# Optimization experiments

Hardware: AMD Instinct MI355X
Metric: run time of the kernel (lower is better)

## Reference

```python
import jax, jax.numpy as jnp
import numpy as np

N, K, D, C, H = 200000, 256, 12, 9, 32
EPS = 1e-8


def setup_inputs() -> dict:
    key = jax.random.key(0)
    ks = jax.random.split(key, 8)
    probe_pos = jax.random.uniform(ks[0], (N, 3), dtype=jnp.float32)
    mu = jax.random.uniform(ks[1], (K, 3), dtype=jnp.float32)
    log_s = jax.random.normal(ks[2], (K, 3), dtype=jnp.float32) * 0.3 - 1.5
    # quaternions near identity (w~1) as in the torch init
    q = jax.random.normal(ks[3], (K, 4), dtype=jnp.float32) * 0.1 + jnp.array([1.0, 0.0, 0.0, 0.0], jnp.float32)
    F = jax.random.normal(ks[4], (K, D), dtype=jnp.float32) * 0.1
    W1 = jax.random.normal(ks[5], (D + 3, H), dtype=jnp.float32) / np.sqrt(D + 3).astype(np.float32)
    b1 = jnp.zeros((H,), jnp.float32)
    W2 = jax.random.normal(ks[6], (H, C), dtype=jnp.float32) / np.sqrt(H).astype(np.float32)
    b2 = jnp.zeros((C,), jnp.float32)
    return {"probe_pos": probe_pos, "mu": mu, "log_s": log_s, "q": q,
            "F": F, "W1": W1, "b1": b1, "W2": W2, "b2": b2}


def quaternion_to_rotation_matrix(q):
    # q: [K,4] (w,x,y,z) -> [K,3,3]
    q = q / (jnp.linalg.norm(q, axis=-1, keepdims=True) + EPS)
    w, x, y, z = q[..., 0], q[..., 1], q[..., 2], q[..., 3]
    r0 = jnp.stack([1 - 2 * y * y - 2 * z * z, 2 * x * y - 2 * w * z, 2 * x * z + 2 * w * y], axis=-1)
    r1 = jnp.stack([2 * x * y + 2 * w * z, 1 - 2 * x * x - 2 * z * z, 2 * y * z - 2 * w * x], axis=-1)
    r2 = jnp.stack([2 * x * z - 2 * w * y, 2 * y * z + 2 * w * x, 1 - 2 * x * x - 2 * y * y], axis=-1)
    return jnp.stack([r0, r1, r2], axis=-2)


def reference(probe_pos, mu, log_s, q, F, W1, b1, W2, b2):
    s = jnp.exp(log_s)                                   # [K,3]
    R = quaternion_to_rotation_matrix(q)                 # [K,3,3]
    s_inv_sq = 1.0 / (s ** 2 + EPS)                      # [K,3]
    # precision = R @ diag(s_inv_sq) @ R^T -> [K,3,3]
    precision = jnp.einsum('kij,kj,klj->kil', R, s_inv_sq, R)
    diff = probe_pos[:, None, :] - mu[None, :, :]        # [N,K,3]
    mahal = jnp.einsum('nki,kij,nkj->nk', diff, precision, diff)  # [N,K]
    gvals = jnp.exp(-0.5 * mahal)                        # [N,K]
    radii = 3.0 * s.max(axis=1)                          # [K]
    dist = jnp.linalg.norm(diff, axis=2)                 # [N,K]
    gvals = gvals * (dist < radii[None, :]).astype(gvals.dtype)
    weights = gvals / (gvals.sum(axis=1, keepdims=True) + EPS)    # [N,K]
    latent = weights @ F                                 # [N,D]
    mlp_in = jnp.concatenate([latent, probe_pos], axis=1)         # [N,D+3]
    h = jax.nn.relu(mlp_in @ W1 + b1)                    # [N,H]
    sh = h @ W2 + b2                                     # [N,C]
    return (sh, latent, weights)
```

## Files before the change

kernel.cpp:

```cpp
#include <hip/hip_runtime.h>

#define KG 256
#define DD 12
#define HH 32
#define CC 9
#define TPB 64
#define KT 32
#define TSTR 36

__global__ __launch_bounds__(256) void gp_pre(
    const float* __restrict__ mu, const float* __restrict__ log_s,
    const float* __restrict__ q, const float* __restrict__ F,
    float* __restrict__ Ct) {
  int k = threadIdx.x;
  if (k >= KG) return;
  float qw = q[k*4+0], qx = q[k*4+1], qy = q[k*4+2], qz = q[k*4+3];
  float nrm = sqrtf(qw*qw + qx*qx + qy*qy + qz*qz);
  float isn = 1.0f / (nrm + 1e-8f);
  qw *= isn; qx *= isn; qy *= isn; qz *= isn;
  float R00 = 1.f - 2.f*(qy*qy + qz*qz);
  float R01 = 2.f*(qx*qy - qw*qz);
  float R02 = 2.f*(qx*qz + qw*qy);
  float R10 = 2.f*(qx*qy + qw*qz);
  float R11 = 1.f - 2.f*(qx*qx + qz*qz);
  float R12 = 2.f*(qy*qz - qw*qx);
  float R20 = 2.f*(qx*qz - qw*qy);
  float R21 = 2.f*(qy*qz + qw*qx);
  float R22 = 1.f - 2.f*(qx*qx + qy*qy);
  float s0 = expf(log_s[k*3+0]);
  float s1 = expf(log_s[k*3+1]);
  float s2 = expf(log_s[k*3+2]);
  float si0 = 1.f/(s0*s0 + 1e-8f);
  float si1 = 1.f/(s1*s1 + 1e-8f);
  float si2 = 1.f/(s2*s2 + 1e-8f);
  float P00 = R00*si0*R00 + R01*si1*R01 + R02*si2*R02;
  float P01 = R00*si0*R10 + R01*si1*R11 + R02*si2*R12;
  float P02 = R00*si0*R20 + R01*si1*R21 + R02*si2*R22;
  float P11 = R10*si0*R10 + R11*si1*R11 + R12*si2*R12;
  float P12 = R10*si0*R20 + R11*si1*R21 + R12*si2*R22;
  float P22 = R20*si0*R20 + R21*si1*R21 + R22*si2*R22;
  float m0 = mu[k*3+0], m1 = mu[k*3+1], m2 = mu[k*3+2];
  float b0 = P00*m0 + P01*m1 + P02*m2;
  float b1v = P01*m0 + P11*m1 + P12*m2;
  float b2v = P02*m0 + P12*m1 + P22*m2;
  float cterm = m0*b0 + m1*b1v + m2*b2v;
  const float f = -0.7213475204444817f;
  float* c = Ct + k*32;
  c[0] = f*P00;  c[1] = f*P11;  c[2] = f*P22;
  c[3] = 2.f*f*P01;  c[4] = 2.f*f*P02;  c[5] = 2.f*f*P12;
  c[6] = -2.f*f*b0;  c[7] = -2.f*f*b1v; c[8] = -2.f*f*b2v;
  c[9] = f*cterm;
  c[10] = -2.f*m0;  c[11] = -2.f*m1;  c[12] = -2.f*m2;
  c[13] = m0*m0 + m1*m1 + m2*m2;
  float smax = fmaxf(s0, fmaxf(s1, s2));
  c[14] = (3.f*smax)*(3.f*smax);
  c[15] = 0.f;
  #pragma unroll
  for (int d = 0; d < DD; ++d) c[16+d] = F[k*DD + d];
  c[28] = c[29] = c[30] = c[31] = 0.f;
}

__device__ __forceinline__ float gauss_eval(
    const float* __restrict__ c,
    float xx, float yy, float zz, float xy, float xz, float yz,
    float x, float y, float z, float pp) {
  float tp = fmaf(c[0], xx, c[9]);
  tp = fmaf(c[1], yy, tp);
  tp = fmaf(c[2], zz, tp);
  tp = fmaf(c[3], xy, tp);
  tp = fmaf(c[4], xz, tp);
  tp = fmaf(c[5], yz, tp);
  tp = fmaf(c[6], x, tp);
  tp = fmaf(c[7], y, tp);
  tp = fmaf(c[8], z, tp);
  float d2 = pp + c[13];
  d2 = fmaf(c[10], x, d2);
  d2 = fmaf(c[11], y, d2);
  d2 = fmaf(c[12], z, d2);
  float e = __builtin_amdgcn_exp2f(tp);
  return (d2 < c[14]) ? e : 0.0f;
}

__global__ __launch_bounds__(TPB) void gp_main(
    const float* __restrict__ pos, const float* __restrict__ Ct,
    const float* __restrict__ W1, const float* __restrict__ b1,
    const float* __restrict__ W2, const float* __restrict__ b2,
    float* __restrict__ sh_out, float* __restrict__ lat_out,
    float* __restrict__ w_out, int N) {
  __shared__ float tile[TPB * TSTR];
  const int lane = threadIdx.x;
  const int pbase = blockIdx.x * TPB;
  const int p = pbase + lane;
  const bool valid = (p < N);
  const int pc = valid ? p : (N - 1);
  const float x = pos[pc*3+0], y = pos[pc*3+1], z = pos[pc*3+2];
  const float xx = x*x, yy = y*y, zz = z*z;
  const float xy = x*y, xz = x*z, yz = y*z;
  const float pp = xx + yy + zz;

  float lat[DD];
  #pragma unroll
  for (int j = 0; j < DD; ++j) lat[j] = 0.0f;
  float denom = 1e-8f;
  #pragma unroll 4
  for (int k = 0; k < KG; ++k) {
    const float* c = Ct + (k << 5);
    float g = gauss_eval(c, xx, yy, zz, xy, xz, yz, x, y, z, pp);
    denom += g;
    #pragma unroll
    for (int j = 0; j < DD; ++j) lat[j] = fmaf(g, c[16+j], lat[j]);
  }
  const float inv = 1.0f / denom;

  float lf[DD];
  #pragma unroll
  for (int j = 0; j < DD; ++j) lf[j] = lat[j] * inv;
  if (valid) {
    float4* lo = (float4*)(lat_out + (size_t)p * DD);
    lo[0] = make_float4(lf[0], lf[1], lf[2],  lf[3]);
    lo[1] = make_float4(lf[4], lf[5], lf[6],  lf[7]);
    lo[2] = make_float4(lf[8], lf[9], lf[10], lf[11]);
  }

  float h[HH];
  #pragma unroll
  for (int j = 0; j < HH; ++j) h[j] = b1[j];
  #pragma unroll
  for (int i = 0; i < DD; ++i) {
    const float v = lf[i];
    #pragma unroll
    for (int j = 0; j < HH; ++j) h[j] = fmaf(v, W1[i*HH + j], h[j]);
  }
  #pragma unroll
  for (int j = 0; j < HH; ++j) h[j] = fmaf(x, W1[12*HH + j], h[j]);
  #pragma unroll
  for (int j = 0; j < HH; ++j) h[j] = fmaf(y, W1[13*HH + j], h[j]);
  #pragma unroll
  for (int j = 0; j < HH; ++j) h[j] = fmaf(z, W1[14*HH + j], h[j]);
  float o[CC];
  #pragma unroll
  for (int c2 = 0; c2 < CC; ++c2) o[c2] = b2[c2];
  #pragma unroll
  for (int j = 0; j < HH; ++j) {
    const float a = fmaxf(h[j], 0.0f);
    #pragma unroll
    for (int c2 = 0; c2 < CC; ++c2) o[c2] = fmaf(a, W2[j*CC + c2], o[c2]);
  }
  if (valid) {
    float* so = sh_out + (size_t)p * CC;
    #pragma unroll
    for (int c2 = 0; c2 < CC; ++c2) so[c2] = o[c2];
  }

  #pragma unroll 1
  for (int k0 = 0; k0 < KG; k0 += KT) {
    #pragma unroll
    for (int kq = 0; kq < KT; kq += 4) {
      float wv[4];
      #pragma unroll
      for (int u = 0; u < 4; ++u) {
        const float* c = Ct + ((k0 + kq + u) << 5);
        wv[u] = gauss_eval(c, xx, yy, zz, xy, xz, yz, x, y, z, pp) * inv;
      }
      *(float4*)&tile[lane*TSTR + kq] = make_float4(wv[0], wv[1], wv[2], wv[3]);
    }
    __syncthreads();
    #pragma unroll
    for (int r4 = 0; r4 < 8; ++r4) {
      const int row = r4*8 + (lane >> 3);
      const int col = (lane & 7) * 4;
      const float4 v = *(const float4*)&tile[row*TSTR + col];
      const int gp2 = pbase + row;
      if (gp2 < N)
        *(float4*)&w_out[(size_t)gp2 * KG + k0 + col] = v;
    }
    __syncthreads();
  }
}

extern "C" void kernel_launch(void* const* d_in, const int* in_sizes, int n_in,
                              void* d_out, int out_size, void* d_ws, size_t ws_size,
                              hipStream_t stream) {
  const float* probe_pos = (const float*)d_in[0];
  const float* mu        = (const float*)d_in[1];
  const float* log_s     = (const float*)d_in[2];
  const float* q         = (const float*)d_in[3];
  const float* F         = (const float*)d_in[4];
  const float* W1        = (const float*)d_in[5];
  const float* b1        = (const float*)d_in[6];
  const float* W2        = (const float*)d_in[7];
  const float* b2        = (const float*)d_in[8];
  const int N = in_sizes[0] / 3;

  float* Ct = (float*)d_ws;
  float* sh_out  = (float*)d_out;
  float* lat_out = sh_out + (size_t)N*CC;
  float* w_out   = lat_out + (size_t)N*DD;

  gp_pre<<<1, 256, 0, stream>>>(mu, log_s, q, F, Ct);
  const int nb = (N + TPB - 1) / TPB;
  gp_main<<<nb, TPB, 0, stream>>>(probe_pos, Ct, W1, b1, W2, b2,
                                  sh_out, lat_out, w_out, N);
}
```

Baseline: 341.2 us.

## Recompute weights with lane-per-Gaussian layout, coefficients in registers, no LDS transpose

The weights pass is restructured so each lane owns four Gaussians, with their coefficients held in registers. The wave then iterates over its 64 points, broadcasting each point's position and inverse denominator through shared memory. Each point's 256-weight row is written as a contiguous, coalesced float4 per lane, which removes the tiled LDS transpose and its per-tile barriers. Block size grows to 256 threads with an occupancy hint. The cost is higher register pressure from the 64-float coefficient cache, which may limit occupancy.

```diff
diff --git a/kernel.cpp b/kernel.cpp
--- a/kernel.cpp
+++ b/kernel.cpp
@@ -4,9 +4,7 @@
 #define DD 12
 #define HH 32
 #define CC 9
-#define TPB 64
-#define KT 32
-#define TSTR 36
+#define TPB 256
 
 __global__ __launch_bounds__(256) void gp_pre(
     const float* __restrict__ mu, const float* __restrict__ log_s,
@@ -81,16 +79,16 @@
   return (d2 < c[14]) ? e : 0.0f;
 }
 
-__global__ __launch_bounds__(TPB) void gp_main(
+__global__ __launch_bounds__(TPB, 4) void gp_main(
     const float* __restrict__ pos, const float* __restrict__ Ct,
     const float* __restrict__ W1, const float* __restrict__ b1,
     const float* __restrict__ W2, const float* __restrict__ b2,
     float* __restrict__ sh_out, float* __restrict__ lat_out,
     float* __restrict__ w_out, int N) {
-  __shared__ float tile[TPB * TSTR];
-  const int lane = threadIdx.x;
+  __shared__ float pxyzi[TPB][4];
+  const int tid = threadIdx.x;
   const int pbase = blockIdx.x * TPB;
-  const int p = pbase + lane;
+  const int p = pbase + tid;
   const bool valid = (p < N);
   const int pc = valid ? p : (N - 1);
   const float x = pos[pc*3+0], y = pos[pc*3+1], z = pos[pc*3+2];
@@ -112,6 +110,8 @@
   }
   const float inv = 1.0f / denom;
 
+  *(float4*)pxyzi[tid] = make_float4(x, y, z, inv);
+
   float lf[DD];
   #pragma unroll
   for (int j = 0; j < DD; ++j) lf[j] = lat[j] * inv;
@@ -122,59 +122,68 @@
     lo[2] = make_float4(lf[8], lf[9], lf[10], lf[11]);
   }
 
-  float h[HH];
-  #pragma unroll
-  for (int j = 0; j < HH; ++j) h[j] = b1[j];
-  #pragma unroll
-  for (int i = 0; i < DD; ++i) {
-    const float v = lf[i];
-    #pragma unroll
-    for (int j = 0; j < HH; ++j) h[j] = fmaf(v, W1[i*HH + j], h[j]);
-  }
-  #pragma unroll
-  for (int j = 0; j < HH; ++j) h[j] = fmaf(x, W1[12*HH + j], h[j]);
-  #pragma unroll
-  for (int j = 0; j < HH; ++j) h[j] = fmaf(y, W1[13*HH + j], h[j]);
-  #pragma unroll
-  for (int j = 0; j < HH; ++j) h[j] = fmaf(z, W1[14*HH + j], h[j]);
-  float o[CC];
-  #pragma unroll
-  for (int c2 = 0; c2 < CC; ++c2) o[c2] = b2[c2];
-  #pragma unroll
-  for (int j = 0; j < HH; ++j) {
-    const float a = fmaxf(h[j], 0.0f);
-    #pragma unroll
-    for (int c2 = 0; c2 < CC; ++c2) o[c2] = fmaf(a, W2[j*CC + c2], o[c2]);
-  }
-  if (valid) {
-    float* so = sh_out + (size_t)p * CC;
-    #pragma unroll
-    for (int c2 = 0; c2 < CC; ++c2) so[c2] = o[c2];
-  }
-
-  #pragma unroll 1
-  for (int k0 = 0; k0 < KG; k0 += KT) {
-    #pragma unroll
-    for (int kq = 0; kq < KT; kq += 4) {
-      float wv[4];
+  {
+    float h[HH];
+    #pragma unroll
+    for (int j = 0; j < HH; ++j) h[j] = b1[j];
+    #pragma unroll
+    for (int i = 0; i < DD; ++i) {
+      const float v = lf[i];
       #pragma unroll
-      for (int u = 0; u < 4; ++u) {
-        const float* c = Ct + ((k0 + kq + u) << 5);
-        wv[u] = gauss_eval(c, xx, yy, zz, xy, xz, yz, x, y, z, pp) * inv;
-      }
-      *(float4*)&tile[lane*TSTR + kq] = make_float4(wv[0], wv[1], wv[2], wv[3]);
+      for (int j = 0; j < HH; ++j) h[j] = fmaf(v, W1[i*HH + j], h[j]);
     }
-    __syncthreads();
-    #pragma unroll
-    for (int r4 = 0; r4 < 8; ++r4) {
-      const int row = r4*8 + (lane >> 3);
-      const int col = (lane & 7) * 4;
-      const float4 v = *(const float4*)&tile[row*TSTR + col];
-      const int gp2 = pbase + row;
-      if (gp2 < N)
-        *(float4*)&w_out[(size_t)gp2 * KG + k0 + col] = v;
+    #pragma unroll
+    for (int j = 0; j < HH; ++j) h[j] = fmaf(x, W1[12*HH + j], h[j]);
+    #pragma unroll
+    for (int j = 0; j < HH; ++j) h[j] = fmaf(y, W1[13*HH + j], h[j]);
+    #pragma unroll
+    for (int j = 0; j < HH; ++j) h[j] = fmaf(z, W1[14*HH + j], h[j]);
+    float o[CC];
+    #pragma unroll
+    for (int c2 = 0; c2 < CC; ++c2) o[c2] = b2[c2];
+    #pragma unroll
+    for (int j = 0; j < HH; ++j) {
+      const float a = fmaxf(h[j], 0.0f);
+      #pragma unroll
+      for (int c2 = 0; c2 < CC; ++c2) o[c2] = fmaf(a, W2[j*CC + c2], o[c2]);
     }
-    __syncthreads();
+    if (valid) {
+      float* so = sh_out + (size_t)p * CC;
+      #pragma unroll
+      for (int c2 = 0; c2 < CC; ++c2) so[c2] = o[c2];
+    }
+  }
+
+  const int lane = tid & 63;
+  const int wbase = tid & ~63;
+  float cb[4][16];
+  #pragma unroll
+  for (int u = 0; u < 4; ++u) {
+    const float4* r = (const float4*)(Ct + (((lane << 2) + u) << 5));
+    *(float4*)&cb[u][0]  = r[0];
+    *(float4*)&cb[u][4]  = r[1];
+    *(float4*)&cb[u][8]  = r[2];
+    *(float4*)&cb[u][12] = r[3];
+  }
+  __syncthreads();
+
+  #pragma unroll 2
+  for (int pi = 0; pi < 64; ++pi) {
+    const int lp = wbase + pi;
+    const float4 b = *(const float4*)pxyzi[lp];
+    const float bx = b.x, by = b.y, bz = b.z, binv = b.w;
+    const float bxx = bx*bx, byy = by*by, bzz = bz*bz;
+    const float bxy = bx*by, bxz = bx*bz, byz = by*bz;
+    const float bpp = bxx + byy + bzz;
+    float wv[4];
+    #pragma unroll
+    for (int u = 0; u < 4; ++u)
+      wv[u] = gauss_eval(cb[u], bxx, byy, bzz, bxy, bxz, byz,
+                         bx, by, bz, bpp) * binv;
+    const int gp2 = pbase + lp;
+    if (gp2 < N)
+      *(float4*)&w_out[(size_t)gp2 * KG + (lane << 2)] =
+          make_float4(wv[0], wv[1], wv[2], wv[3]);
   }
 }
 
```

Result: faster. 315.0 us (-7.7%).
